# Kernel tuning notes

Hardware: AMD Instinct MI355X
Metric: run time of the kernel (lower is better)

Reference implementation:

```python
import jax, jax.numpy as jnp
import numpy as np

EDGE_WIDTH = 25
NUM_ROTATIONS = 6
VISITATION_SCALE = 0.5
B = 1024
EMB = 128


def _shuffle_to_egocentric(x, rot):
    # x: [B, 6, H, W]; rot: [B] int. out[b, j] = x[b, (j - rot[b]) % 6]
    idx = (jnp.arange(NUM_ROTATIONS)[None, :] - rot[:, None]) % NUM_ROTATIONS  # [B,6]
    return jnp.take_along_axis(x, idx[:, :, None, None], axis=1)


def setup_inputs() -> dict:
    key = jax.random.key(0)
    ks = jax.random.split(key, 11)
    H = EDGE_WIDTH
    return {
        "embedded_static": jax.random.normal(ks[0], (B, EMB, H, H), jnp.float32),
        "embedded_dynamic": jax.random.normal(ks[1], (B, EMB, H, H), jnp.float32),
        "obstacle_mask": jax.random.uniform(ks[2], (B, H, H), jnp.float32),
        "observability_current": jax.random.uniform(ks[3], (B, H, H), jnp.float32),
        "observability_in_memory": jax.random.uniform(ks[4], (B, H, H), jnp.float32),
        "previous_visitations": jax.random.uniform(ks[5], (B, NUM_ROTATIONS, H, H), jnp.float32),
        "all_previous_targets": jax.random.uniform(ks[6], (B, NUM_ROTATIONS, H, H), jnp.float32),
        "previous_target": jax.random.uniform(ks[7], (B, NUM_ROTATIONS, H, H), jnp.float32),
        "leader_location": jax.random.uniform(ks[8], (B, H, H), jnp.float32),
        "follower_location": jax.random.uniform(ks[9], (B, H, H), jnp.float32),
        "rotations": jax.random.randint(ks[10], (B,), 0, NUM_ROTATIONS, jnp.int32),
    }


def reference(embedded_static, embedded_dynamic, obstacle_mask,
              observability_current, observability_in_memory,
              previous_visitations, all_previous_targets, previous_target,
              leader_location, follower_location, rotations):
    H = EDGE_WIDTH
    # non-hierarchical: sum static + dynamic embeddings
    embedded_env = embedded_static + embedded_dynamic  # [B, EMB, H, H]

    obs_mem = observability_in_memory[:, None]  # [B,1,H,H]
    prev_vis_scaled = previous_visitations * VISITATION_SCALE
    all_prev_tgt = all_previous_targets * VISITATION_SCALE
    prev_tgt = previous_target  # note: original scales only all_previous_targets by 0.5

    # egocentric circular shift of rotation channels (vectorized gather)
    prev_vis_scaled = _shuffle_to_egocentric(prev_vis_scaled, rotations)
    all_prev_tgt = _shuffle_to_egocentric(all_prev_tgt, rotations)
    prev_tgt = _shuffle_to_egocentric(prev_tgt, rotations)

    # sum over rotation channels of the UNSCALED raw visitations (as in original)
    all_visitations = jnp.sum(previous_visitations, axis=1, keepdims=True)

    embedded = jnp.concatenate((
        embedded_env,
        obstacle_mask[:, None],
        observability_current[:, None],
        obs_mem,
        prev_vis_scaled,
        all_visitations,
        leader_location[:, None],
        follower_location[:, None],
    ), axis=1)

    all_pos_prev = jnp.sum(all_prev_tgt, axis=1, keepdims=True)
    pos_prev = jnp.sum(prev_tgt, axis=1, keepdims=True)
    embedded = jnp.concatenate((embedded, all_prev_tgt, prev_tgt, all_pos_prev, pos_prev), axis=1)

    environment_tensor = embedded * obs_mem

    # utility channels: constant ones channel + compass one-hot rotation planes
    Bn = environment_tensor.shape[0]
    env_channel = jnp.ones((Bn, 1, H, H), environment_tensor.dtype)
    compass = jax.nn.one_hot(rotations, NUM_ROTATIONS, dtype=environment_tensor.dtype)
    compass = jnp.broadcast_to(compass[:, :, None, None], (Bn, NUM_ROTATIONS, H, H))
    return jnp.concatenate((environment_tensor, env_channel, compass), axis=1)
```

## Files before the change

### kernel.cpp

```cpp
#include <hip/hip_runtime.h>
#include <stdint.h>

#define HW 625
#define NROT 6
#define C_OUT 161
#define OUT_PER_B (C_OUT * HW)
#define IN_PER_B  (128 * HW)
#define NT 256

__global__ __launch_bounds__(NT)
void env_embed(const float* __restrict__ sta, const float* __restrict__ dyn,
               const float* __restrict__ obst, const float* __restrict__ ocur,
               const float* __restrict__ omem, const float* __restrict__ pvis,
               const float* __restrict__ atgt, const float* __restrict__ ptgt,
               const float* __restrict__ lead, const float* __restrict__ foll,
               const int* __restrict__ rots, float* __restrict__ out)
{
    const int b = blockIdx.x;
    const int t = threadIdx.x;
    const int rot = rots[b];
    __shared__ float lds_obs[HW];

    const int bHW = b * HW;
    float* const out_b = out + (size_t)b * OUT_PER_B;

    for (int p = t; p < HW; p += NT) {
        const float obs = omem[bHW + p];
        lds_obs[p] = obs;
        float* const ob = out_b + p;

        ob[128 * HW] = obst[bHW + p] * obs;
        ob[129 * HW] = ocur[bHW + p] * obs;
        ob[130 * HW] = obs * obs;
        ob[138 * HW] = lead[bHW + p] * obs;
        ob[139 * HW] = foll[bHW + p] * obs;

        float s_pv = 0.f, s_at = 0.f, s_pt = 0.f;
        #pragma unroll
        for (int r = 0; r < NROT; ++r) {
            const float pv = pvis[(b * NROT + r) * HW + p];
            const float at = atgt[(b * NROT + r) * HW + p];
            const float pt = ptgt[(b * NROT + r) * HW + p];
            s_pv += pv; s_at += at; s_pt += pt;
            int j = r + rot; if (j >= NROT) j -= NROT;
            ob[(131 + j) * HW] = pv * 0.5f * obs;
            ob[(140 + j) * HW] = at * 0.5f * obs;
            ob[(146 + j) * HW] = pt * obs;
        }
        ob[137 * HW] = s_pv * obs;
        ob[152 * HW] = s_at * 0.5f * obs;
        ob[153 * HW] = s_pt * obs;
        ob[154 * HW] = 1.0f;
        #pragma unroll
        for (int j = 0; j < NROT; ++j)
            ob[(155 + j) * HW] = (j == rot) ? 1.0f : 0.0f;
    }

    __syncthreads();

    const float* const sb = sta + (size_t)b * IN_PER_B;
    const float* const db = dyn + (size_t)b * IN_PER_B;
    const int amode = b & 3;

    for (int k = t; k < IN_PER_B / 4; k += NT) {
        const int idx = 4 * k;
        const float4 s4 = *(const float4*)(sb + idx);
        const float4 d4 = *(const float4*)(db + idx);

        int q = idx % 625;
        const float o0 = lds_obs[q]; q = (q + 1 == HW) ? 0 : q + 1;
        const float o1 = lds_obs[q]; q = (q + 1 == HW) ? 0 : q + 1;
        const float o2 = lds_obs[q]; q = (q + 1 == HW) ? 0 : q + 1;
        const float o3 = lds_obs[q];

        const float r0 = (s4.x + d4.x) * o0;
        const float r1 = (s4.y + d4.y) * o1;
        const float r2 = (s4.z + d4.z) * o2;
        const float r3 = (s4.w + d4.w) * o3;

        float* const po = out_b + idx;
        if (amode == 0) {
            *(float4*)po = make_float4(r0, r1, r2, r3);
        } else if (amode == 2) {
            *(float2*)po       = make_float2(r0, r1);
            *(float2*)(po + 2) = make_float2(r2, r3);
        } else {
            po[0] = r0; po[1] = r1; po[2] = r2; po[3] = r3;
        }
    }
}

extern "C" void kernel_launch(void* const* d_in, const int* in_sizes, int n_in,
                              void* d_out, int out_size, void* d_ws, size_t ws_size,
                              hipStream_t stream) {
    const float* sta  = (const float*)d_in[0];
    const float* dyn  = (const float*)d_in[1];
    const float* obst = (const float*)d_in[2];
    const float* ocur = (const float*)d_in[3];
    const float* omem = (const float*)d_in[4];
    const float* pvis = (const float*)d_in[5];
    const float* atgt = (const float*)d_in[6];
    const float* ptgt = (const float*)d_in[7];
    const float* lead = (const float*)d_in[8];
    const float* foll = (const float*)d_in[9];
    const int*   rots = (const int*)d_in[10];
    float* out = (float*)d_out;

    const int nb = in_sizes[10];

    hipLaunchKernelGGL(env_embed, dim3(nb), dim3(NT), 0, stream,
                       sta, dyn, obst, ocur, omem, pvis, atgt, ptgt,
                       lead, foll, rots, out);
}
```

Baseline: 252.1 us.

## Split per-batch work into separate small-channel and quarter-slice embedding blocks

```diff
diff --git a/kernel.cpp b/kernel.cpp
--- a/kernel.cpp
+++ b/kernel.cpp
@@ -7,6 +7,9 @@
 #define OUT_PER_B (C_OUT * HW)
 #define IN_PER_B  (128 * HW)
 #define NT 256
+#define QF  20000
+#define NF4 5000
+#define CST 629
 
 __global__ __launch_bounds__(NT)
 void env_embed(const float* __restrict__ sta, const float* __restrict__ dyn,
@@ -14,80 +17,113 @@
                const float* __restrict__ omem, const float* __restrict__ pvis,
                const float* __restrict__ atgt, const float* __restrict__ ptgt,
                const float* __restrict__ lead, const float* __restrict__ foll,
-               const int* __restrict__ rots, float* __restrict__ out)
+               const int* __restrict__ rots, float* __restrict__ out, const int nb)
 {
-    const int b = blockIdx.x;
+    const int bid = blockIdx.x;
     const int t = threadIdx.x;
-    const int rot = rots[b];
-    __shared__ float lds_obs[HW];
 
-    const int bHW = b * HW;
-    float* const out_b = out + (size_t)b * OUT_PER_B;
+    if (bid < nb) {
+        const int b = bid;
+        const int rot = rots[b];
+        const int bHW = b * HW;
+        float* const out_b = out + (size_t)b * OUT_PER_B;
 
-    for (int p = t; p < HW; p += NT) {
-        const float obs = omem[bHW + p];
-        lds_obs[p] = obs;
-        float* const ob = out_b + p;
+        for (int p = t; p < HW; p += NT) {
+            const float obs = omem[bHW + p];
+            float* const ob = out_b + p;
 
-        ob[128 * HW] = obst[bHW + p] * obs;
-        ob[129 * HW] = ocur[bHW + p] * obs;
-        ob[130 * HW] = obs * obs;
-        ob[138 * HW] = lead[bHW + p] * obs;
-        ob[139 * HW] = foll[bHW + p] * obs;
+            ob[128 * HW] = obst[bHW + p] * obs;
+            ob[129 * HW] = ocur[bHW + p] * obs;
+            ob[130 * HW] = obs * obs;
+            ob[138 * HW] = lead[bHW + p] * obs;
+            ob[139 * HW] = foll[bHW + p] * obs;
 
-        float s_pv = 0.f, s_at = 0.f, s_pt = 0.f;
-        #pragma unroll
-        for (int r = 0; r < NROT; ++r) {
-            const float pv = pvis[(b * NROT + r) * HW + p];
-            const float at = atgt[(b * NROT + r) * HW + p];
-            const float pt = ptgt[(b * NROT + r) * HW + p];
-            s_pv += pv; s_at += at; s_pt += pt;
-            int j = r + rot; if (j >= NROT) j -= NROT;
-            ob[(131 + j) * HW] = pv * 0.5f * obs;
-            ob[(140 + j) * HW] = at * 0.5f * obs;
-            ob[(146 + j) * HW] = pt * obs;
+            float s_pv = 0.f, s_at = 0.f, s_pt = 0.f;
+            #pragma unroll
+            for (int r = 0; r < NROT; ++r) {
+                const float pv = pvis[(b * NROT + r) * HW + p];
+                const float at = atgt[(b * NROT + r) * HW + p];
+                const float pt = ptgt[(b * NROT + r) * HW + p];
+                s_pv += pv; s_at += at; s_pt += pt;
+                int jj = r + rot; if (jj >= NROT) jj -= NROT;
+                ob[(131 + jj) * HW] = pv * 0.5f * obs;
+                ob[(140 + jj) * HW] = at * 0.5f * obs;
+                ob[(146 + jj) * HW] = pt * obs;
+            }
+            ob[137 * HW] = s_pv * obs;
+            ob[152 * HW] = s_at * 0.5f * obs;
+            ob[153 * HW] = s_pt * obs;
+            ob[154 * HW] = 1.0f;
+            #pragma unroll
+            for (int jj = 0; jj < NROT; ++jj)
+                ob[(155 + jj) * HW] = (jj == rot) ? 1.0f : 0.0f;
         }
-        ob[137 * HW] = s_pv * obs;
-        ob[152 * HW] = s_at * 0.5f * obs;
-        ob[153 * HW] = s_pt * obs;
-        ob[154 * HW] = 1.0f;
-        #pragma unroll
-        for (int j = 0; j < NROT; ++j)
-            ob[(155 + j) * HW] = (j == rot) ? 1.0f : 0.0f;
+        return;
     }
 
+    const int hb = bid - nb;
+    const int b = hb >> 2;
+    const int j = hb & 3;
+
+    __shared__ float lobs[4 * CST];
+    for (int p = t; p < HW; p += NT) {
+        const float v = omem[b * HW + p];
+        lobs[p] = v; lobs[CST + p] = v; lobs[2 * CST + p] = v; lobs[3 * CST + p] = v;
+    }
     __syncthreads();
 
-    const float* const sb = sta + (size_t)b * IN_PER_B;
-    const float* const db = dyn + (size_t)b * IN_PER_B;
+    const float* const sb = sta + (size_t)b * IN_PER_B + j * QF;
+    const float* const db = dyn + (size_t)b * IN_PER_B + j * QF;
+    float* const ob = out + (size_t)b * OUT_PER_B + j * QF;
+    const float* const L = lobs + ((t >> 3) & 3) * CST;
     const int amode = b & 3;
 
-    for (int k = t; k < IN_PER_B / 4; k += NT) {
-        const int idx = 4 * k;
-        const float4 s4 = *(const float4*)(sb + idx);
-        const float4 d4 = *(const float4*)(db + idx);
+#define OBS4(Q, O0, O1, O2, O3) {                                  \
+        int qq = (Q);                                              \
+        O0 = L[qq]; qq = (qq == HW - 1) ? 0 : qq + 1;              \
+        O1 = L[qq]; qq = (qq == HW - 1) ? 0 : qq + 1;              \
+        O2 = L[qq]; qq = (qq == HW - 1) ? 0 : qq + 1;              \
+        O3 = L[qq]; }
 
-        int q = idx % 625;
-        const float o0 = lds_obs[q]; q = (q + 1 == HW) ? 0 : q + 1;
-        const float o1 = lds_obs[q]; q = (q + 1 == HW) ? 0 : q + 1;
-        const float o2 = lds_obs[q]; q = (q + 1 == HW) ? 0 : q + 1;
-        const float o3 = lds_obs[q];
+#define STORE4(PO, R0, R1, R2, R3) {                               \
+        if (amode == 0)       *(float4*)(PO) = make_float4(R0, R1, R2, R3); \
+        else if (amode == 2) { *(float2*)(PO) = make_float2(R0, R1);        \
+                               *(float2*)((PO) + 2) = make_float2(R2, R3); }\
+        else { (PO)[0] = R0; (PO)[1] = R1; (PO)[2] = R2; (PO)[3] = R3; } }
 
-        const float r0 = (s4.x + d4.x) * o0;
-        const float r1 = (s4.y + d4.y) * o1;
-        const float r2 = (s4.z + d4.z) * o2;
-        const float r3 = (s4.w + d4.w) * o3;
+    int k = t;
+    for (; k + NT < NF4; k += 2 * NT) {
+        const int kB = k + NT;
+        const int iA = 4 * k, iB = 4 * kB;
+        const float4 sA = *(const float4*)(sb + iA);
+        const float4 dA = *(const float4*)(db + iA);
+        const float4 sB = *(const float4*)(sb + iB);
+        const float4 dB = *(const float4*)(db + iB);
 
-        float* const po = out_b + idx;
-        if (amode == 0) {
-            *(float4*)po = make_float4(r0, r1, r2, r3);
-        } else if (amode == 2) {
-            *(float2*)po       = make_float2(r0, r1);
-            *(float2*)(po + 2) = make_float2(r2, r3);
-        } else {
-            po[0] = r0; po[1] = r1; po[2] = r2; po[3] = r3;
-        }
+        float a0, a1, a2, a3, b0, b1, b2, b3;
+        OBS4(iA % HW, a0, a1, a2, a3);
+        OBS4(iB % HW, b0, b1, b2, b3);
+
+        const float rA0 = (sA.x + dA.x) * a0, rA1 = (sA.y + dA.y) * a1;
+        const float rA2 = (sA.z + dA.z) * a2, rA3 = (sA.w + dA.w) * a3;
+        const float rB0 = (sB.x + dB.x) * b0, rB1 = (sB.y + dB.y) * b1;
+        const float rB2 = (sB.z + dB.z) * b2, rB3 = (sB.w + dB.w) * b3;
+
+        STORE4(ob + iA, rA0, rA1, rA2, rA3);
+        STORE4(ob + iB, rB0, rB1, rB2, rB3);
     }
+    if (k < NF4) {
+        const int iA = 4 * k;
+        const float4 sA = *(const float4*)(sb + iA);
+        const float4 dA = *(const float4*)(db + iA);
+        float a0, a1, a2, a3;
+        OBS4(iA % HW, a0, a1, a2, a3);
+        const float rA0 = (sA.x + dA.x) * a0, rA1 = (sA.y + dA.y) * a1;
+        const float rA2 = (sA.z + dA.z) * a2, rA3 = (sA.w + dA.w) * a3;
+        STORE4(ob + iA, rA0, rA1, rA2, rA3);
+    }
+#undef OBS4
+#undef STORE4
 }
 
 extern "C" void kernel_launch(void* const* d_in, const int* in_sizes, int n_in,
@@ -108,7 +144,7 @@
 
     const int nb = in_sizes[10];
 
-    hipLaunchKernelGGL(env_embed, dim3(nb), dim3(NT), 0, stream,
+    hipLaunchKernelGGL(env_embed, dim3(5 * nb), dim3(NT), 0, stream,
                        sta, dyn, obst, ocur, omem, pvis, atgt, ptgt,
-                       lead, foll, rots, out);
+                       lead, foll, rots, out, nb);
 }
```

After: 240.9 us. 4.4% less time.
